# Optimization experiments

Measured on AMD Instinct MI355X. Metric: run time of the kernel, lower is better.

Reference implementation:

```python
import jax, jax.numpy as jnp
import numpy as np

H = 2880      # hidden_size
I = 2880      # intermediate_size
E = 8         # num_experts
K = 4         # experts_per_token
N = 1024      # num tokens
EPS = 1e-5
ALPHA = 1.702
BETA = 1.0


def setup_inputs() -> dict:
    key = jax.random.key(0)
    ks = jax.random.split(key, 8)
    s = 0.02
    return {
        "x": jax.random.normal(ks[0], (N, H), jnp.float32),
        "norm_w": jnp.ones((H,), jnp.float32),
        "gate_w": jax.random.normal(ks[1], (E, H), jnp.float32) * s,
        "gate_b": jax.random.normal(ks[2], (E,), jnp.float32) * s,
        "w_gate_up": jax.random.normal(ks[3], (E, 2 * I, H), jnp.float32) * s,
        "b_gate_up": jax.random.normal(ks[4], (E, 2 * I), jnp.float32) * s,
        "w_down": jax.random.normal(ks[5], (E, H, I), jnp.float32) * s,
        "b_down": jax.random.normal(ks[6], (E, H), jnp.float32) * s,
    }


def reference(x, norm_w, gate_w, gate_b, w_gate_up, b_gate_up, w_down, b_down):
    # RMSNorm
    t = x * jax.lax.rsqrt(jnp.mean(x * x, axis=-1, keepdims=True) + EPS) * norm_w
    # Router gate (Linear with bias)
    logits = t @ gate_w.T + gate_b                      # [N, E]
    # Renormalize routing: top-k of logits, softmax over selected logits
    top_vals, top_idx = jax.lax.top_k(logits, K)        # [N, K]
    route_w = jax.nn.softmax(top_vals, axis=-1)         # [N, K]
    # Dense combine matrix [N, E] (zero for unselected experts)
    n_ar = jnp.arange(N)[:, None]
    R = jnp.zeros((N, E), t.dtype).at[n_ar, top_idx].add(route_w)
    # Fused gate_up projection per expert: [E, N, 2I]
    h = jnp.einsum('nh,eih->eni', t, w_gate_up) + b_gate_up[:, None, :]
    x_glu, x_lin = h[..., :I], h[..., I:]
    # SwiGLU with per-expert alpha/beta (all 1.702 / 1.0)
    act = x_glu * jax.nn.sigmoid(ALPHA * x_glu) * (x_lin + BETA)   # [E, N, I]
    # Down projection per expert: [E, N, H]
    outs = jnp.einsum('eni,ehi->enh', act, w_down) + b_down[:, None, :]
    # Weighted combine over selected experts + residual
    y = jnp.einsum('ne,enh->nh', R, outs)
    return x + y
```

## Files before the change

### kernel.cpp

```cpp
#include <hip/hip_runtime.h>
#include <hip/hip_bf16.h>

#define NTOK 1024
#define HDIM 2880
#define IDIM 2880
#define NEXP 8
#define BK 64
#define NT 45

typedef __attribute__((ext_vector_type(4))) float fx4;
typedef __attribute__((ext_vector_type(8))) short sx8;
typedef __attribute__((ext_vector_type(8))) unsigned short usx8;

typedef const __attribute__((address_space(1))) void* gas_p;
typedef __attribute__((address_space(3))) void* las_p;

__device__ __forceinline__ unsigned short f2bf(float f) {
  __hip_bfloat16 b = __float2bfloat16(f);
  return __builtin_bit_cast(unsigned short, b);
}
__device__ __forceinline__ usx8 cvt8(fx4 a, fx4 b) {
  usx8 u = {f2bf(a.x), f2bf(a.y), f2bf(a.z), f2bf(a.w),
            f2bf(b.x), f2bf(b.y), f2bf(b.z), f2bf(b.w)};
  return u;
}

#define MFMA16(a, b, c) __builtin_amdgcn_mfma_f32_16x16x32_bf16(a, b, c, 0, 0, 0)

__global__ __launch_bounds__(256) void init_out_k(const float* __restrict__ x,
                                                  float* __restrict__ out) {
  int i = blockIdx.x * 256 + threadIdx.x;
  ((fx4*)out)[i] = ((const fx4*)x)[i];
}

__global__ __launch_bounds__(256) void cvt_bf_k(const float* __restrict__ src,
                                                unsigned short* __restrict__ dst,
                                                long n8) {
  const long stride = (long)gridDim.x * 256;
  for (long i = (long)blockIdx.x * 256 + threadIdx.x; i < n8; i += stride) {
    fx4 a = *(const fx4*)(src + i * 8);
    fx4 b = *(const fx4*)(src + i * 8 + 4);
    *(usx8*)(dst + i * 8) = cvt8(a, b);
  }
}

__global__ __launch_bounds__(256) void rms_router_k(
    const float* __restrict__ x, const float* __restrict__ norm_w,
    const float* __restrict__ gate_w, const float* __restrict__ gate_b,
    unsigned short* __restrict__ t_bf, int* __restrict__ cnt,
    int* __restrict__ tok, float* __restrict__ wgt) {
  const int n = blockIdx.x;
  const int tid = threadIdx.x;
  const int wid = tid >> 6, lane = tid & 63;
  const float* xr = x + (size_t)n * HDIM;

  float ss = 0.f;
  for (int h = tid; h < HDIM; h += 256) { float v = xr[h]; ss += v * v; }
  #pragma unroll
  for (int o = 32; o > 0; o >>= 1) ss += __shfl_down(ss, o);
  __shared__ float sred[4];
  if (lane == 0) sred[wid] = ss;
  __syncthreads();
  const float rstd =
      rsqrtf((sred[0] + sred[1] + sred[2] + sred[3]) * (1.0f / HDIM) + 1e-5f);

  float p[NEXP];
  #pragma unroll
  for (int e = 0; e < NEXP; e++) p[e] = 0.f;
  for (int h = tid; h < HDIM; h += 256) {
    float xv = xr[h] * norm_w[h];
    t_bf[(size_t)n * HDIM + h] = f2bf(xv * rstd);
    #pragma unroll
    for (int e = 0; e < NEXP; e++) p[e] += xv * gate_w[e * HDIM + h];
  }
  __shared__ float pls[4][NEXP];
  #pragma unroll
  for (int e = 0; e < NEXP; e++) {
    float v = p[e];
    #pragma unroll
    for (int o = 32; o > 0; o >>= 1) v += __shfl_down(v, o);
    if (lane == 0) pls[wid][e] = v;
  }
  __syncthreads();
  if (tid == 0) {
    float lg[NEXP];
    #pragma unroll
    for (int e = 0; e < NEXP; e++)
      lg[e] = (pls[0][e] + pls[1][e] + pls[2][e] + pls[3][e]) * rstd + gate_b[e];
    unsigned used = 0;
    float val[4];
    int idx[4];
    for (int k = 0; k < 4; k++) {
      float best = -1e30f;
      int bi = 0;
      for (int e = 0; e < NEXP; e++)
        if (!((used >> e) & 1u) && lg[e] > best) { best = lg[e]; bi = e; }
      used |= 1u << bi;
      val[k] = best;
      idx[k] = bi;
    }
    float sum = 0.f, w[4];
    for (int k = 0; k < 4; k++) { w[k] = expf(val[k] - val[0]); sum += w[k]; }
    for (int k = 0; k < 4; k++) {
      int e = idx[k];
      int slot = atomicAdd(&cnt[e], 1);
      tok[e * NTOK + slot] = n;
      wgt[e * NTOK + slot] = w[k] / sum;
    }
  }
}

template <bool BF16B>
__global__ __launch_bounds__(256, 3) void gemm1_k(
    const unsigned short* __restrict__ t_bf,
    const unsigned short* __restrict__ wgu_bf,
    const float* __restrict__ w_gate_up, const float* __restrict__ b_gate_up,
    const int* __restrict__ cnt, const int* __restrict__ tok,
    unsigned short* __restrict__ act_bf) {
  const int h = blockIdx.x;
  const int g = h >> 6, z = (h >> 3) & 7, v = h & 7;
  const int u = g * 8 + v;
  const int e = u / 45;
  const int c0 = (u % 45) * 64;
  const int m0 = z * 128;
  const int ce = cnt[e];
  if (m0 >= ce) return;

  const int tid = threadIdx.x, lane = tid & 63, wid = tid >> 6;
  const int fr = lane & 15, fq = lane >> 4;
  const int wm = wid >> 1, wn = wid & 1;
  const int sw = ((lane & 7) ^ ((lane >> 3) & 7)) * 8;

  __shared__ __align__(16) unsigned short Ash[128 * 64];
  __shared__ __align__(16) unsigned short Bsh[128 * 64];

  const fx4 FZ = {0.f, 0.f, 0.f, 0.f};
  fx4 accG[4][2], accL[4][2];
  #pragma unroll
  for (int m = 0; m < 4; m++)
    #pragma unroll
    for (int n = 0; n < 2; n++) { accG[m][n] = FZ; accL[m][n] = FZ; }

  const unsigned short* gA[4];
  #pragma unroll
  for (int j = 0; j < 4; ++j) {
    int R = m0 + wid * 32 + j * 8 + (lane >> 3);
    int rc = R < ce ? R : ce - 1;
    gA[j] = t_bf + (size_t)tok[e * NTOK + rc] * HDIM + sw;
  }
  const unsigned short* gB[4];
  #pragma unroll
  for (int j = 0; j < 4; ++j) {
    int br = wid * 32 + j * 8 + (lane >> 3);
    int wr = br < 64 ? (c0 + br) : (IDIM + c0 + (br - 64));
    gB[j] = wgu_bf + ((size_t)e * (2 * IDIM) + wr) * HDIM + sw;
  }
  const float* fB[4];
  int fRow[4], fCh[4];
  if constexpr (!BF16B) {
    #pragma unroll
    for (int q = 0; q < 4; ++q) {
      int s = tid + 256 * q;
      fRow[q] = s >> 3;
      fCh[q] = s & 7;
      int wr = fRow[q] < 64 ? (c0 + fRow[q]) : (IDIM + c0 + (fRow[q] - 64));
      fB[q] = w_gate_up + ((size_t)e * (2 * IDIM) + wr) * HDIM + fCh[q] * 8;
    }
  }

  for (int t = 0; t < NT; ++t) {
    const int ko = t * BK;
    __syncthreads();
    #pragma unroll
    for (int j = 0; j < 4; ++j)
      __builtin_amdgcn_global_load_lds((gas_p)(gA[j] + ko),
                                       (las_p)&Ash[(wid * 32 + j * 8) * 64], 16,
                                       0, 0);
    if constexpr (BF16B) {
      #pragma unroll
      for (int j = 0; j < 4; ++j)
        __builtin_amdgcn_global_load_lds((gas_p)(gB[j] + ko),
                                         (las_p)&Bsh[(wid * 32 + j * 8) * 64],
                                         16, 0, 0);
    } else {
      #pragma unroll
      for (int q = 0; q < 4; ++q) {
        fx4 a = *(const fx4*)(fB[q] + ko);
        fx4 b = *(const fx4*)(fB[q] + ko + 4);
        *(usx8*)&Bsh[fRow[q] * 64 + ((fCh[q] ^ (fRow[q] & 7)) * 8)] = cvt8(a, b);
      }
    }
    __syncthreads();
    #pragma unroll
    for (int ks = 0; ks < 2; ++ks) {
      const int rc = ks * 4 + fq;
      sx8 aF[4], bG[2], bL[2];
      #pragma unroll
      for (int m = 0; m < 4; ++m)
        aF[m] = *(const sx8*)&Ash[(wm * 64 + m * 16 + fr) * 64 +
                                  ((rc ^ (fr & 7)) * 8)];
      #pragma unroll
      for (int n = 0; n < 2; ++n) {
        bG[n] = *(const sx8*)&Bsh[(wn * 32 + n * 16 + fr) * 64 +
                                  ((rc ^ (fr & 7)) * 8)];
        bL[n] = *(const sx8*)&Bsh[(64 + wn * 32 + n * 16 + fr) * 64 +
                                  ((rc ^ (fr & 7)) * 8)];
      }
      #pragma unroll
      for (int n = 0; n < 2; ++n)
        #pragma unroll
        for (int m = 0; m < 4; ++m) {
          accG[m][n] = MFMA16(aF[m], bG[n], accG[m][n]);
          accL[m][n] = MFMA16(aF[m], bL[n], accL[m][n]);
        }
    }
  }

  #pragma unroll
  for (int n = 0; n < 2; ++n) {
    const int col = c0 + wn * 32 + n * 16 + fr;
    const float bg = b_gate_up[e * (2 * IDIM) + col];
    const float bl = b_gate_up[e * (2 * IDIM) + IDIM + col];
    #pragma unroll
    for (int m = 0; m < 4; ++m) {
      #pragma unroll
      for (int r = 0; r < 4; ++r) {
        int slot = m0 + wm * 64 + m * 16 + fq * 4 + r;
        if (slot < ce) {
          float gv = accG[m][n][r] + bg;
          float lv = accL[m][n][r] + bl;
          float a = gv * (1.0f / (1.0f + __expf(-1.702f * gv))) * (lv + 1.0f);
          act_bf[((size_t)e * NTOK + slot) * IDIM + col] = f2bf(a);
        }
      }
    }
  }
}

template <bool BF16B>
__global__ __launch_bounds__(256, 3) void gemm2_k(
    const unsigned short* __restrict__ act_bf,
    const unsigned short* __restrict__ wd_bf, const float* __restrict__ w_down,
    const float* __restrict__ b_down, const int* __restrict__ cnt,
    const int* __restrict__ tok, const float* __restrict__ wgt,
    float* __restrict__ out) {
  const int h = blockIdx.x;
  const int g = h >> 6, z = (h >> 3) & 7, v = h & 7;
  const int u = g * 8 + v;
  const int e = u / 30;
  const int c0 = (u % 30) * 96;
  const int m0 = z * 128;
  const int ce = cnt[e];
  if (m0 >= ce) return;

  const int tid = threadIdx.x, lane = tid & 63, wid = tid >> 6;
  const int fr = lane & 15, fq = lane >> 4;
  const int wm = wid >> 1, wn = wid & 1;
  const int sw = ((lane & 7) ^ ((lane >> 3) & 7)) * 8;

  __shared__ __align__(16) unsigned short Ash[128 * 64];
  __shared__ __align__(16) unsigned short Bsh[96 * 64];

  const fx4 FZ = {0.f, 0.f, 0.f, 0.f};
  fx4 acc[4][3];
  #pragma unroll
  for (int m = 0; m < 4; m++)
    #pragma unroll
    for (int n = 0; n < 3; n++) acc[m][n] = FZ;

  const unsigned short* gA[4];
  #pragma unroll
  for (int j = 0; j < 4; ++j) {
    int R = m0 + wid * 32 + j * 8 + (lane >> 3);
    int rc = R < ce ? R : ce - 1;
    gA[j] = act_bf + ((size_t)e * NTOK + rc) * IDIM + sw;
  }
  const unsigned short* gB[3];
  #pragma unroll
  for (int j = 0; j < 3; ++j) {
    int br = wid * 24 + j * 8 + (lane >> 3);
    gB[j] = wd_bf + ((size_t)e * HDIM + c0 + br) * IDIM + sw;
  }
  const float* fB[3];
  int fRow[3], fCh[3];
  if constexpr (!BF16B) {
    #pragma unroll
    for (int q = 0; q < 3; ++q) {
      int s = tid + 256 * q;
      fRow[q] = s >> 3;
      fCh[q] = s & 7;
      fB[q] = w_down + ((size_t)e * HDIM + c0 + fRow[q]) * IDIM + fCh[q] * 8;
    }
  }

  for (int t = 0; t < NT; ++t) {
    const int ko = t * BK;
    __syncthreads();
    #pragma unroll
    for (int j = 0; j < 4; ++j)
      __builtin_amdgcn_global_load_lds((gas_p)(gA[j] + ko),
                                       (las_p)&Ash[(wid * 32 + j * 8) * 64], 16,
                                       0, 0);
    if constexpr (BF16B) {
      #pragma unroll
      for (int j = 0; j < 3; ++j)
        __builtin_amdgcn_global_load_lds((gas_p)(gB[j] + ko),
                                         (las_p)&Bsh[(wid * 24 + j * 8) * 64],
                                         16, 0, 0);
    } else {
      #pragma unroll
      for (int q = 0; q < 3; ++q) {
        fx4 a = *(const fx4*)(fB[q] + ko);
        fx4 b = *(const fx4*)(fB[q] + ko + 4);
        *(usx8*)&Bsh[fRow[q] * 64 + ((fCh[q] ^ (fRow[q] & 7)) * 8)] = cvt8(a, b);
      }
    }
    __syncthreads();
    #pragma unroll
    for (int ks = 0; ks < 2; ++ks) {
      const int rc = ks * 4 + fq;
      sx8 aF[4], bB[3];
      #pragma unroll
      for (int m = 0; m < 4; ++m)
        aF[m] = *(const sx8*)&Ash[(wm * 64 + m * 16 + fr) * 64 +
                                  ((rc ^ (fr & 7)) * 8)];
      #pragma unroll
      for (int n = 0; n < 3; ++n)
        bB[n] = *(const sx8*)&Bsh[(wn * 48 + n * 16 + fr) * 64 +
                                  ((rc ^ (fr & 7)) * 8)];
      #pragma unroll
      for (int n = 0; n < 3; ++n)
        #pragma unroll
        for (int m = 0; m < 4; ++m)
          acc[m][n] = MFMA16(aF[m], bB[n], acc[m][n]);
    }
  }

  #pragma unroll
  for (int n = 0; n < 3; ++n) {
    const int col = c0 + wn * 48 + n * 16 + fr;
    const float bias = b_down[e * HDIM + col];
    #pragma unroll
    for (int m = 0; m < 4; ++m) {
      #pragma unroll
      for (int r = 0; r < 4; ++r) {
        int slot = m0 + wm * 64 + m * 16 + fq * 4 + r;
        if (slot < ce) {
          int token = tok[e * NTOK + slot];
          float w = wgt[e * NTOK + slot];
          atomicAdd(&out[(size_t)token * HDIM + col], w * (acc[m][n][r] + bias));
        }
      }
    }
  }
}

extern "C" void kernel_launch(void* const* d_in, const int* in_sizes, int n_in,
                              void* d_out, int out_size, void* d_ws,
                              size_t ws_size, hipStream_t stream) {
  const float* x = (const float*)d_in[0];
  const float* norm_w = (const float*)d_in[1];
  const float* gate_w = (const float*)d_in[2];
  const float* gate_b = (const float*)d_in[3];
  const float* w_gate_up = (const float*)d_in[4];
  const float* b_gate_up = (const float*)d_in[5];
  const float* w_down = (const float*)d_in[6];
  const float* b_down = (const float*)d_in[7];
  float* out = (float*)d_out;

  char* ws = (char*)d_ws;
  size_t off = 0;
  unsigned short* t_bf = (unsigned short*)(ws + off);
  off += (size_t)NTOK * HDIM * 2;
  unsigned short* act_bf = (unsigned short*)(ws + off);
  off += (size_t)NEXP * NTOK * IDIM * 2;
  int* cnt = (int*)(ws + off);
  off += 256;
  int* tok = (int*)(ws + off);
  off += (size_t)NEXP * NTOK * 4;
  float* wgt = (float*)(ws + off);
  off += (size_t)NEXP * NTOK * 4;

  const size_t WD_E = (size_t)NEXP * HDIM * IDIM;
  const size_t WGU_E = (size_t)NEXP * 2 * IDIM * HDIM;
  unsigned short* wd_bf = (unsigned short*)(ws + off);
  const bool haveWd = (off + WD_E * 2) <= ws_size;
  if (haveWd) off += WD_E * 2;
  unsigned short* wgu_bf = (unsigned short*)(ws + off);
  const bool haveWgu = (off + WGU_E * 2) <= ws_size;

  hipMemsetAsync(cnt, 0, NEXP * sizeof(int), stream);
  init_out_k<<<2880, 256, 0, stream>>>(x, out);
  if (haveWgu)
    cvt_bf_k<<<4096, 256, 0, stream>>>(w_gate_up, wgu_bf, (long)(WGU_E / 8));
  if (haveWd)
    cvt_bf_k<<<4096, 256, 0, stream>>>(w_down, wd_bf, (long)(WD_E / 8));
  rms_router_k<<<NTOK, 256, 0, stream>>>(x, norm_w, gate_w, gate_b, t_bf, cnt,
                                         tok, wgt);
  if (haveWgu)
    gemm1_k<true><<<2880, 256, 0, stream>>>(t_bf, wgu_bf, w_gate_up, b_gate_up,
                                            cnt, tok, act_bf);
  else
    gemm1_k<false><<<2880, 256, 0, stream>>>(t_bf, nullptr, w_gate_up,
                                             b_gate_up, cnt, tok, act_bf);
  if (haveWd)
    gemm2_k<true><<<1920, 256, 0, stream>>>(act_bf, wd_bf, w_down, b_down, cnt,
                                            tok, wgt, out);
  else
    gemm2_k<false><<<1920, 256, 0, stream>>>(act_bf, nullptr, w_down, b_down,
                                             cnt, tok, wgt, out);
}
```

Measured before the change: 671.0 us.

## Double-buffer LDS and enlarge GEMM tiles to 256-row blocks of 512 threads

Both expert GEMMs move to 512-thread blocks with 256-row M tiles and wider N tiles: 96+96 gate/lin columns in gemm1 and 192 columns in gemm2. The LDS buffers are doubled so the next K-slice loads are issued before computing on the current one, with s_setprio raised around the MFMA bursts. This aims to hide global-load latency and raise data reuse per block, at the cost of more LDS and registers per block. Each thread still computes a 4x3 or 4x6 fragment set. The per-thread index math (wid ranges 0-7) may no longer match the unchanged wm/wn mapping, which could leave coverage gaps.

Measured after the change: 912.2 us. 1.36x slower.

```diff
diff --git a/kernel.cpp b/kernel.cpp
--- a/kernel.cpp
+++ b/kernel.cpp
@@ -26,6 +26,7 @@
 }
 
 #define MFMA16(a, b, c) __builtin_amdgcn_mfma_f32_16x16x32_bf16(a, b, c, 0, 0, 0)
+#define VMCNT0 asm volatile("s_waitcnt vmcnt(0)" ::: "memory")
 
 __global__ __launch_bounds__(256) void init_out_k(const float* __restrict__ x,
                                                   float* __restrict__ out) {
@@ -111,18 +112,18 @@
 }
 
 template <bool BF16B>
-__global__ __launch_bounds__(256, 3) void gemm1_k(
+__global__ __launch_bounds__(512, 2) void gemm1_k(
     const unsigned short* __restrict__ t_bf,
     const unsigned short* __restrict__ wgu_bf,
     const float* __restrict__ w_gate_up, const float* __restrict__ b_gate_up,
     const int* __restrict__ cnt, const int* __restrict__ tok,
     unsigned short* __restrict__ act_bf) {
   const int h = blockIdx.x;
-  const int g = h >> 6, z = (h >> 3) & 7, v = h & 7;
+  const int g = h >> 5, z = (h >> 3) & 3, v = h & 7;
   const int u = g * 8 + v;
-  const int e = u / 45;
-  const int c0 = (u % 45) * 64;
-  const int m0 = z * 128;
+  const int e = u / 30;
+  const int c0 = (u % 30) * 96;
+  const int m0 = z * 256;
   const int ce = cnt[e];
   if (m0 >= ce) return;
 
@@ -131,15 +132,15 @@
   const int wm = wid >> 1, wn = wid & 1;
   const int sw = ((lane & 7) ^ ((lane >> 3) & 7)) * 8;
 
-  __shared__ __align__(16) unsigned short Ash[128 * 64];
-  __shared__ __align__(16) unsigned short Bsh[128 * 64];
+  __shared__ __align__(16) unsigned short Ash[2][256 * 64];
+  __shared__ __align__(16) unsigned short Bsh[2][192 * 64];
 
   const fx4 FZ = {0.f, 0.f, 0.f, 0.f};
-  fx4 accG[4][2], accL[4][2];
+  fx4 accG[4][3], accL[4][3];
   #pragma unroll
   for (int m = 0; m < 4; m++)
     #pragma unroll
-    for (int n = 0; n < 2; n++) { accG[m][n] = FZ; accL[m][n] = FZ; }
+    for (int n = 0; n < 3; n++) { accG[m][n] = FZ; accL[m][n] = FZ; }
 
   const unsigned short* gA[4];
   #pragma unroll
@@ -148,77 +149,110 @@
     int rc = R < ce ? R : ce - 1;
     gA[j] = t_bf + (size_t)tok[e * NTOK + rc] * HDIM + sw;
   }
-  const unsigned short* gB[4];
-  #pragma unroll
-  for (int j = 0; j < 4; ++j) {
-    int br = wid * 32 + j * 8 + (lane >> 3);
-    int wr = br < 64 ? (c0 + br) : (IDIM + c0 + (br - 64));
+  const unsigned short* gB[3];
+  #pragma unroll
+  for (int j = 0; j < 3; ++j) {
+    int br = wid * 24 + j * 8 + (lane >> 3);
+    int wr = br < 96 ? (c0 + br) : (IDIM + c0 + (br - 96));
     gB[j] = wgu_bf + ((size_t)e * (2 * IDIM) + wr) * HDIM + sw;
   }
-  const float* fB[4];
-  int fRow[4], fCh[4];
+  const float* fB[3];
+  int fRow[3], fCh[3];
   if constexpr (!BF16B) {
     #pragma unroll
-    for (int q = 0; q < 4; ++q) {
-      int s = tid + 256 * q;
+    for (int q = 0; q < 3; ++q) {
+      int s = tid + 512 * q;
       fRow[q] = s >> 3;
       fCh[q] = s & 7;
-      int wr = fRow[q] < 64 ? (c0 + fRow[q]) : (IDIM + c0 + (fRow[q] - 64));
+      int wr = fRow[q] < 96 ? (c0 + fRow[q]) : (IDIM + c0 + (fRow[q] - 96));
       fB[q] = w_gate_up + ((size_t)e * (2 * IDIM) + wr) * HDIM + fCh[q] * 8;
     }
   }
 
+  fx4 Ra[6];
+  #define G1_DMA_A(kt, bb)                                                     \
+    {                                                                          \
+      _Pragma("unroll") for (int j = 0; j < 4; ++j)                            \
+          __builtin_amdgcn_global_load_lds(                                    \
+              (gas_p)(gA[j] + (size_t)(kt)*BK),                                \
+              (las_p)&Ash[bb][(wid * 32 + j * 8) * 64], 16, 0, 0);             \
+    }
+  #define G1_DMA_B(kt, bb)                                                     \
+    {                                                                          \
+      _Pragma("unroll") for (int j = 0; j < 3; ++j)                            \
+          __builtin_amdgcn_global_load_lds(                                    \
+              (gas_p)(gB[j] + (size_t)(kt)*BK),                                \
+              (las_p)&Bsh[bb][(wid * 24 + j * 8) * 64], 16, 0, 0);             \
+    }
+  #define G1_FLOAD(kt)                                                         \
+    {                                                                          \
+      _Pragma("unroll") for (int q = 0; q < 3; ++q) {                          \
+        Ra[2 * q] = *(const fx4*)(fB[q] + (size_t)(kt)*BK);                    \
+        Ra[2 * q + 1] = *(const fx4*)(fB[q] + (size_t)(kt)*BK + 4);            \
+      }                                                                        \
+    }
+  #define G1_FWRITE(bb)                                                        \
+    {                                                                          \
+      _Pragma("unroll") for (int q = 0; q < 3; ++q)                            \
+          *(usx8*)&Bsh[bb][fRow[q] * 64 + ((fCh[q] ^ (fRow[q] & 7)) * 8)] =    \
+              cvt8(Ra[2 * q], Ra[2 * q + 1]);                                  \
+    }
+  #define G1_COMPUTE(bb)                                                       \
+    {                                                                          \
+      _Pragma("unroll") for (int ks = 0; ks < 2; ++ks) {                       \
+        const int rk = ks * 4 + fq;                                            \
+        sx8 aF[4], bG[3], bL[3];                                               \
+        _Pragma("unroll") for (int m = 0; m < 4; ++m) aF[m] =                  \
+            *(const sx8*)&Ash[bb][(wm * 64 + m * 16 + fr) * 64 +               \
+                                  ((rk ^ (fr & 7)) * 8)];                      \
+        _Pragma("unroll") for (int n = 0; n < 3; ++n) {                        \
+          bG[n] = *(const sx8*)&Bsh[bb][(wn * 48 + n * 16 + fr) * 64 +         \
+                                        ((rk ^ (fr & 7)) * 8)];                \
+          bL[n] = *(const sx8*)&Bsh[bb][(96 + wn * 48 + n * 16 + fr) * 64 +    \
+                                        ((rk ^ (fr & 7)) * 8)];                \
+        }                                                                      \
+        __builtin_amdgcn_s_setprio(1);                                         \
+        _Pragma("unroll") for (int n = 0; n < 3; ++n)                          \
+            _Pragma("unroll") for (int m = 0; m < 4; ++m) {                    \
+          accG[m][n] = MFMA16(aF[m], bG[n], accG[m][n]);                       \
+          accL[m][n] = MFMA16(aF[m], bL[n], accL[m][n]);                       \
+        }                                                                      \
+        __builtin_amdgcn_s_setprio(0);                                         \
+      }                                                                        \
+    }
+
+  G1_DMA_A(0, 0);
+  if constexpr (BF16B) {
+    G1_DMA_B(0, 0);
+  } else {
+    G1_FLOAD(0);
+    G1_FWRITE(0);
+  }
+  VMCNT0;
+  __syncthreads();
+
+  int p = 0;
   for (int t = 0; t < NT; ++t) {
-    const int ko = t * BK;
+    if (t + 1 < NT) {
+      G1_DMA_A(t + 1, p ^ 1);
+      if constexpr (BF16B) {
+        G1_DMA_B(t + 1, p ^ 1);
+      } else {
+        G1_FLOAD(t + 1);
+      }
+    }
+    G1_COMPUTE(p);
+    if constexpr (!BF16B) {
+      if (t + 1 < NT) G1_FWRITE(p ^ 1);
+    }
+    VMCNT0;
     __syncthreads();
-    #pragma unroll
-    for (int j = 0; j < 4; ++j)
-      __builtin_amdgcn_global_load_lds((gas_p)(gA[j] + ko),
-                                       (las_p)&Ash[(wid * 32 + j * 8) * 64], 16,
-                                       0, 0);
-    if constexpr (BF16B) {
-      #pragma unroll
-      for (int j = 0; j < 4; ++j)
-        __builtin_amdgcn_global_load_lds((gas_p)(gB[j] + ko),
-                                         (las_p)&Bsh[(wid * 32 + j * 8) * 64],
-                                         16, 0, 0);
-    } else {
-      #pragma unroll
-      for (int q = 0; q < 4; ++q) {
-        fx4 a = *(const fx4*)(fB[q] + ko);
-        fx4 b = *(const fx4*)(fB[q] + ko + 4);
-        *(usx8*)&Bsh[fRow[q] * 64 + ((fCh[q] ^ (fRow[q] & 7)) * 8)] = cvt8(a, b);
-      }
-    }
-    __syncthreads();
-    #pragma unroll
-    for (int ks = 0; ks < 2; ++ks) {
-      const int rc = ks * 4 + fq;
-      sx8 aF[4], bG[2], bL[2];
-      #pragma unroll
-      for (int m = 0; m < 4; ++m)
-        aF[m] = *(const sx8*)&Ash[(wm * 64 + m * 16 + fr) * 64 +
-                                  ((rc ^ (fr & 7)) * 8)];
-      #pragma unroll
-      for (int n = 0; n < 2; ++n) {
-        bG[n] = *(const sx8*)&Bsh[(wn * 32 + n * 16 + fr) * 64 +
-                                  ((rc ^ (fr & 7)) * 8)];
-        bL[n] = *(const sx8*)&Bsh[(64 + wn * 32 + n * 16 + fr) * 64 +
-                                  ((rc ^ (fr & 7)) * 8)];
-      }
-      #pragma unroll
-      for (int n = 0; n < 2; ++n)
-        #pragma unroll
-        for (int m = 0; m < 4; ++m) {
-          accG[m][n] = MFMA16(aF[m], bG[n], accG[m][n]);
-          accL[m][n] = MFMA16(aF[m], bL[n], accL[m][n]);
-        }
-    }
-  }
-
-  #pragma unroll
-  for (int n = 0; n < 2; ++n) {
-    const int col = c0 + wn * 32 + n * 16 + fr;
+    p ^= 1;
+  }
+
+  #pragma unroll
+  for (int n = 0; n < 3; ++n) {
+    const int col = c0 + wn * 48 + n * 16 + fr;
     const float bg = b_gate_up[e * (2 * IDIM) + col];
     const float bl = b_gate_up[e * (2 * IDIM) + IDIM + col];
     #pragma unroll
@@ -238,18 +272,18 @@
 }
 
 template <bool BF16B>
-__global__ __launch_bounds__(256, 3) void gemm2_k(
+__global__ __launch_bounds__(512, 2) void gemm2_k(
     const unsigned short* __restrict__ act_bf,
     const unsigned short* __restrict__ wd_bf, const float* __restrict__ w_down,
     const float* __restrict__ b_down, const int* __restrict__ cnt,
     const int* __restrict__ tok, const float* __restrict__ wgt,
     float* __restrict__ out) {
   const int h = blockIdx.x;
-  const int g = h >> 6, z = (h >> 3) & 7, v = h & 7;
+  const int g = h >> 5, z = (h >> 3) & 3, v = h & 7;
   const int u = g * 8 + v;
-  const int e = u / 30;
-  const int c0 = (u % 30) * 96;
-  const int m0 = z * 128;
+  const int e = u / 15;
+  const int c0 = (u % 15) * 192;
+  const int m0 = z * 256;
   const int ce = cnt[e];
   if (m0 >= ce) return;
 
@@ -258,15 +292,15 @@
   const int wm = wid >> 1, wn = wid & 1;
   const int sw = ((lane & 7) ^ ((lane >> 3) & 7)) * 8;
 
-  __shared__ __align__(16) unsigned short Ash[128 * 64];
-  __shared__ __align__(16) unsigned short Bsh[96 * 64];
+  __shared__ __align__(16) unsigned short Ash[2][256 * 64];
+  __shared__ __align__(16) unsigned short Bsh[2][192 * 64];
 
   const fx4 FZ = {0.f, 0.f, 0.f, 0.f};
-  fx4 acc[4][3];
+  fx4 acc[4][6];
   #pragma unroll
   for (int m = 0; m < 4; m++)
     #pragma unroll
-    for (int n = 0; n < 3; n++) acc[m][n] = FZ;
+    for (int n = 0; n < 6; n++) acc[m][n] = FZ;
 
   const unsigned short* gA[4];
   #pragma unroll
@@ -286,59 +320,92 @@
   if constexpr (!BF16B) {
     #pragma unroll
     for (int q = 0; q < 3; ++q) {
-      int s = tid + 256 * q;
+      int s = tid + 512 * q;
       fRow[q] = s >> 3;
       fCh[q] = s & 7;
       fB[q] = w_down + ((size_t)e * HDIM + c0 + fRow[q]) * IDIM + fCh[q] * 8;
     }
   }
 
+  fx4 Ra[6];
+  #define G2_DMA_A(kt, bb)                                                     \
+    {                                                                          \
+      _Pragma("unroll") for (int j = 0; j < 4; ++j)                            \
+          __builtin_amdgcn_global_load_lds(                                    \
+              (gas_p)(gA[j] + (size_t)(kt)*BK),                                \
+              (las_p)&Ash[bb][(wid * 32 + j * 8) * 64], 16, 0, 0);             \
+    }
+  #define G2_DMA_B(kt, bb)                                                     \
+    {                                                                          \
+      _Pragma("unroll") for (int j = 0; j < 3; ++j)                            \
+          __builtin_amdgcn_global_load_lds(                                    \
+              (gas_p)(gB[j] + (size_t)(kt)*BK),                                \
+              (las_p)&Bsh[bb][(wid * 24 + j * 8) * 64], 16, 0, 0);             \
+    }
+  #define G2_FLOAD(kt)                                                         \
+    {                                                                          \
+      _Pragma("unroll") for (int q = 0; q < 3; ++q) {                          \
+        Ra[2 * q] = *(const fx4*)(fB[q] + (size_t)(kt)*BK);                    \
+        Ra[2 * q + 1] = *(const fx4*)(fB[q] + (size_t)(kt)*BK + 4);            \
+      }                                                                        \
+    }
+  #define G2_FWRITE(bb)                                                        \
+    {                                                                          \
+      _Pragma("unroll") for (int q = 0; q < 3; ++q)                            \
+          *(usx8*)&Bsh[bb][fRow[q] * 64 + ((fCh[q] ^ (fRow[q] & 7)) * 8)] =    \
+              cvt8(Ra[2 * q], Ra[2 * q + 1]);                                  \
+    }
+  #define G2_COMPUTE(bb)                                                       \
+    {                                                                          \
+      _Pragma("unroll") for (int ks = 0; ks < 2; ++ks) {                       \
+        const int rk = ks * 4 + fq;                                            \
+        sx8 aF[4], bB[6];                                                      \
+        _Pragma("unroll") for (int m = 0; m < 4; ++m) aF[m] =                  \
+            *(const sx8*)&Ash[bb][(wm * 64 + m * 16 + fr) * 64 +               \
+                                  ((rk ^ (fr & 7)) * 8)];                      \
+        _Pragma("unroll") for (int n = 0; n < 6; ++n) bB[n] =                  \
+            *(const sx8*)&Bsh[bb][(wn * 96 + n * 16 + fr) * 64 +               \
+                                  ((rk ^ (fr & 7)) * 8)];                      \
+        __builtin_amdgcn_s_setprio(1);                                         \
+        _Pragma("unroll") for (int n = 0; n < 6; ++n)                          \
+            _Pragma("unroll") for (int m = 0; m < 4; ++m)                      \
+                acc[m][n] = MFMA16(aF[m], bB[n], acc[m][n]);                   \
+        __builtin_amdgcn_s_setprio(0);                                         \
+      }                                                                        \
+    }
+
+  G2_DMA_A(0, 0);
+  if constexpr (BF16B) {
+    G2_DMA_B(0, 0);
+  } else {
+    G2_FLOAD(0);
+    G2_FWRITE(0);
+  }
+  VMCNT0;
+  __syncthreads();
+
+  int p = 0;
   for (int t = 0; t < NT; ++t) {
-    const int ko = t * BK;
+    if (t + 1 < NT) {
+      G2_DMA_A(t + 1, p ^ 1);
+      if constexpr (BF16B) {
+        G2_DMA_B(t + 1, p ^ 1);
+      } else {
+        G2_FLOAD(t + 1);
+      }
+    }
+    G2_COMPUTE(p);
+    if constexpr (!BF16B) {
+      if (t + 1 < NT) G2_FWRITE(p ^ 1);
+    }
+    VMCNT0;
     __syncthreads();
-    #pragma unroll
-    for (int j = 0; j < 4; ++j)
-      __builtin_amdgcn_global_load_lds((gas_p)(gA[j] + ko),
-                                       (las_p)&Ash[(wid * 32 + j * 8) * 64], 16,
-                                       0, 0);
-    if constexpr (BF16B) {
-      #pragma unroll
-      for (int j = 0; j < 3; ++j)
-        __builtin_amdgcn_global_load_lds((gas_p)(gB[j] + ko),
-                                         (las_p)&Bsh[(wid * 24 + j * 8) * 64],
-                                         16, 0, 0);
-    } else {
-      #pragma unroll
-      for (int q = 0; q < 3; ++q) {
-        fx4 a = *(const fx4*)(fB[q] + ko);
-        fx4 b = *(const fx4*)(fB[q] + ko + 4);
-        *(usx8*)&Bsh[fRow[q] * 64 + ((fCh[q] ^ (fRow[q] & 7)) * 8)] = cvt8(a, b);
-      }
-    }
-    __syncthreads();
-    #pragma unroll
-    for (int ks = 0; ks < 2; ++ks) {
-      const int rc = ks * 4 + fq;
-      sx8 aF[4], bB[3];
-      #pragma unroll
-      for (int m = 0; m < 4; ++m)
-        aF[m] = *(const sx8*)&Ash[(wm * 64 + m * 16 + fr) * 64 +
-                                  ((rc ^ (fr & 7)) * 8)];
-      #pragma unroll
-      for (int n = 0; n < 3; ++n)
-        bB[n] = *(const sx8*)&Bsh[(wn * 48 + n * 16 + fr) * 64 +
-                                  ((rc ^ (fr & 7)) * 8)];
-      #pragma unroll
-      for (int n = 0; n < 3; ++n)
-        #pragma unroll
-        for (int m = 0; m < 4; ++m)
-          acc[m][n] = MFMA16(aF[m], bB[n], acc[m][n]);
-    }
-  }
-
-  #pragma unroll
-  for (int n = 0; n < 3; ++n) {
-    const int col = c0 + wn * 48 + n * 16 + fr;
+    p ^= 1;
+  }
+
+  #pragma unroll
+  for (int n = 0; n < 6; ++n) {
+    const int col = c0 + wn * 96 + n * 16 + fr;
     const float bias = b_down[e * HDIM + col];
     #pragma unroll
     for (int m = 0; m < 4; ++m) {
@@ -398,15 +465,15 @@
   rms_router_k<<<NTOK, 256, 0, stream>>>(x, norm_w, gate_w, gate_b, t_bf, cnt,
                                          tok, wgt);
   if (haveWgu)
-    gemm1_k<true><<<2880, 256, 0, stream>>>(t_bf, wgu_bf, w_gate_up, b_gate_up,
-                                            cnt, tok, act_bf);
+    gemm1_k<true><<<960, 512, 0, stream>>>(t_bf, wgu_bf, w_gate_up, b_gate_up,
+                                           cnt, tok, act_bf);
   else
-    gemm1_k<false><<<2880, 256, 0, stream>>>(t_bf, nullptr, w_gate_up,
-                                             b_gate_up, cnt, tok, act_bf);
+    gemm1_k<false><<<960, 512, 0, stream>>>(t_bf, nullptr, w_gate_up,
+                                            b_gate_up, cnt, tok, act_bf);
   if (haveWd)
-    gemm2_k<true><<<1920, 256, 0, stream>>>(act_bf, wd_bf, w_down, b_down, cnt,
-                                            tok, wgt, out);
+    gemm2_k<true><<<480, 512, 0, stream>>>(act_bf, wd_bf, w_down, b_down, cnt,
+                                           tok, wgt, out);
   else
-    gemm2_k<false><<<1920, 256, 0, stream>>>(act_bf, nullptr, w_down, b_down,
-                                             cnt, tok, wgt, out);
-}
+    gemm2_k<false><<<480, 512, 0, stream>>>(act_bf, nullptr, w_down, b_down,
+                                            cnt, tok, wgt, out);
+}
```
